# Performance work log

Hardware: AMD Instinct MI355X
Metric: run time of the kernel (lower is better)

The kernel has to match this reference:

```python
import jax, jax.numpy as jnp
import numpy as np

B, N, D, E, FF, TOP_K = 4, 1024, 1024, 8, 4096, 2

def setup_inputs() -> dict:
    key = jax.random.key(0)
    ks = jax.random.split(key, 6)
    s = lambda k, shape: (jax.random.normal(k, shape, jnp.float32) * 0.02)
    x  = jax.random.normal(ks[0], (B, N, D), jnp.float32)
    Wr = s(ks[1], (E, D))            # router: logits = x @ Wr.T (no bias)
    W1 = s(ks[2], (E, D, FF)); b1 = jnp.zeros((E, FF), jnp.float32)  # fc1
    Wg = s(ks[3], (E, D, FF)); bg = jnp.zeros((E, FF), jnp.float32)  # fc_gate
    W2 = s(ks[4], (E, FF, D)); b2 = jnp.zeros((E, D), jnp.float32)   # fc2
    return {"x": x, "Wr": Wr, "W1": W1, "b1": b1, "Wg": Wg, "bg": bg, "W2": W2, "b2": b2}

def reference(x, Wr, W1, b1, Wg, bg, W2, b2):
    Bb, Nn, Dd = x.shape
    xf = x.reshape(-1, Dd)                      # [T, D]
    T = xf.shape[0]
    logits = xf @ Wr.T                          # [T, E]
    probs = jax.nn.softmax(logits, axis=-1)
    topv, topi = jax.lax.top_k(probs, TOP_K)    # [T, K]
    topv = topv / (topv.sum(-1, keepdims=True) + 1e-6)
    # per-(expert,token) combine weight: comb[t, e] = sum_k topv[t,k] * (topi[t,k]==e)
    comb = jnp.zeros((T, E), x.dtype).at[jnp.arange(T)[:, None], topi].add(topv)
    # scan over experts (fixed small E) to keep memory to one [T, FF] at a time
    def step(acc, p):
        w1, bb1, wg, bbg, w2, bb2, we = p       # we: [T]
        h = xf @ w1 + bb1                       # [T, FF]
        g = xf @ wg + bbg
        out = (jax.nn.silu(g) * h) @ w2 + bb2   # [T, D]
        return acc + we[:, None] * out, None
    acc, _ = jax.lax.scan(step, jnp.zeros((T, Dd), x.dtype), (W1, b1, Wg, bg, W2, b2, comb.T))
    out_final = acc.reshape(Bb, Nn, Dd)
    # load-balance aux loss (computed under no_grad in torch)
    counts = jnp.zeros((E,), x.dtype).at[topi.reshape(-1)].add(1.0)
    frac = counts / (counts.sum() + 1e-6)
    lb = jax.lax.stop_gradient((frac * probs.sum(0)).sum() * E)
    return out_final, lb
```

## Files before the change

kernel.cpp:

```cpp
#include <hip/hip_runtime.h>
#include <hip/hip_bf16.h>
#include <math.h>

#define T_TOK 4096
#define D_DIM 1024
#define E_EXP 8
#define FF_DIM 4096
#define NROWS (T_TOK * 2)
#define MAXT1 40
#define MAXT2 72

typedef unsigned short u16;
typedef unsigned int u32;
typedef __attribute__((ext_vector_type(8))) short bf16x8;
typedef __attribute__((ext_vector_type(4))) float f32x4;
typedef __attribute__((ext_vector_type(2))) unsigned int u32x2;
typedef __attribute__((ext_vector_type(4))) short s16x4;

__device__ __forceinline__ u16 f2bf(float f) {
    union { float f; unsigned u; } v; v.f = f;
    unsigned r = v.u + 0x7FFFu + ((v.u >> 16) & 1u);
    return (u16)(r >> 16);
}

typedef const __attribute__((address_space(1))) u32* gas1_t;
typedef __attribute__((address_space(3))) u32* las3_t;
#define GLOAD16(g, l) __builtin_amdgcn_global_load_lds((gas1_t)(const void*)(g), (las3_t)(void*)(l), 16, 0, 0)
#define MFMA(a, b, c) __builtin_amdgcn_mfma_f32_16x16x32_bf16((a), (b), (c), 0, 0, 0)
#define CVTPK(dst, lo, hi) asm("v_cvt_pk_bf16_f32 %0, %1, %2" : "=v"(dst) : "v"(lo), "v"(hi))
#define CFENCE() asm volatile("" ::: "memory")
#define SIGB(r) (((r) ^ ((r) >> 2)) & 7)


__global__ __launch_bounds__(256) void k_router(
    const float* __restrict__ x, const float* __restrict__ Wr,
    u16* __restrict__ xbf,
    int* __restrict__ tok_e, float* __restrict__ tok_w,
    int* __restrict__ cnt, float* __restrict__ probsum)
{
    __shared__ float bp[E_EXP];
    __shared__ int   bc[E_EXP];
    const int tid = threadIdx.x;
    if (tid < E_EXP) { bp[tid] = 0.f; bc[tid] = 0; }
    __syncthreads();
    const int wave = tid >> 6, lane = tid & 63;
    const int t = blockIdx.x * 4 + wave;
    const float* xt = x + (size_t)t * D_DIM;
    u16* xo = xbf + (size_t)t * D_DIM;
    float a[E_EXP] = {0.f,0.f,0.f,0.f,0.f,0.f,0.f,0.f};
    for (int j = lane; j < D_DIM; j += 64) {
        float xv = xt[j];
        xo[j] = f2bf(xv);
        #pragma unroll
        for (int e = 0; e < E_EXP; e++) a[e] = fmaf(xv, Wr[e * D_DIM + j], a[e]);
    }
    #pragma unroll
    for (int e = 0; e < E_EXP; e++) {
        #pragma unroll
        for (int off = 32; off; off >>= 1) a[e] += __shfl_xor(a[e], off, 64);
    }
    if (lane == 0) {
        float mx = a[0];
        #pragma unroll
        for (int e = 1; e < E_EXP; e++) mx = fmaxf(mx, a[e]);
        float p[E_EXP], s = 0.f;
        #pragma unroll
        for (int e = 0; e < E_EXP; e++) { p[e] = expf(a[e] - mx); s += p[e]; }
        float inv = 1.f / s;
        #pragma unroll
        for (int e = 0; e < E_EXP; e++) { p[e] *= inv; atomicAdd(&bp[e], p[e]); }
        int e0 = 0; float v0 = p[0];
        #pragma unroll
        for (int e = 1; e < E_EXP; e++) if (p[e] > v0) { v0 = p[e]; e0 = e; }
        int e1 = -1; float v1 = -1.f;
        #pragma unroll
        for (int e = 0; e < E_EXP; e++) if (e != e0 && p[e] > v1) { v1 = p[e]; e1 = e; }
        float sv = v0 + v1 + 1e-6f;
        tok_e[2*t] = e0; tok_e[2*t+1] = e1;
        tok_w[2*t] = v0 / sv; tok_w[2*t+1] = v1 / sv;
        atomicAdd(&bc[e0], 1); atomicAdd(&bc[e1], 1);
    }
    __syncthreads();
    if (tid < E_EXP) { atomicAdd(&cnt[tid], bc[tid]); atomicAdd(&probsum[tid], bp[tid]); }
}

__global__ void k_prefix(const int* __restrict__ cnt, const float* __restrict__ probsum,
                         int* __restrict__ basep, int* __restrict__ cursor,
                         float* __restrict__ out_lb,
                         int* __restrict__ nt1, int* __restrict__ te1, int* __restrict__ tm1,
                         int* __restrict__ nt2, int* __restrict__ te2, int* __restrict__ tm2)
{
    if (threadIdx.x == 0) {
        int b = 0; float lb = 0.f;
        for (int e = 0; e < E_EXP; e++) {
            basep[e] = b; b += cnt[e];
            lb += ((float)cnt[e] / (8192.f + 1e-6f)) * probsum[e];
        }
        *out_lb = lb * (float)E_EXP;
        int n1 = 0, n2 = 0;
        for (int e = 0; e < E_EXP; e++) {
            for (int m = 0; m < cnt[e]; m += 256) { te1[n1] = e; tm1[n1] = m; n1++; }
            for (int m = 0; m < cnt[e]; m += 128) { te2[n2] = e; tm2[n2] = m; n2++; }
        }
        *nt1 = n1; *nt2 = n2;
    }
    if (threadIdx.x < E_EXP) cursor[threadIdx.x] = 0;
}

__global__ void k_assign(const int* __restrict__ tok_e, const float* __restrict__ tok_w,
                         const int* __restrict__ basep, int* __restrict__ cursor,
                         int* __restrict__ row_token, int* __restrict__ row_slot,
                         float* __restrict__ row_weight)
{
    int t = blockIdx.x * blockDim.x + threadIdx.x;
    if (t >= T_TOK) return;
    #pragma unroll
    for (int k = 0; k < 2; k++) {
        int e = tok_e[2*t + k];
        int pos = basep[e] + atomicAdd(&cursor[e], 1);
        row_token[pos] = t; row_slot[pos] = k; row_weight[pos] = tok_w[2*t + k];
    }
}

__global__ __launch_bounds__(256) void k_cvt_w2(const float* __restrict__ W2, u16* __restrict__ w2t,
                                                int* __restrict__ cnt, float* __restrict__ probsum) {
    __shared__ u16 t[64][68];
    if (blockIdx.x == 0 && blockIdx.y == 0 && blockIdx.z == 0 && threadIdx.x < E_EXP) {
        cnt[threadIdx.x] = 0; probsum[threadIdx.x] = 0.f;
    }
    const float* in = W2 + (size_t)blockIdx.z * FF_DIM * D_DIM;
    u16* out = w2t + (size_t)blockIdx.z * FF_DIM * D_DIM;
    const int R = FF_DIM, C = D_DIM;
    const int r0 = blockIdx.y * 64, c0 = blockIdx.x * 64;
    const int tid = threadIdx.x;
    const int lr = tid >> 4, lc = (tid & 15) * 4;
    #pragma unroll
    for (int i = 0; i < 4; i++) {
        const int r = lr + i * 16;
        f32x4 v = *(const f32x4*)(in + (size_t)(r0 + r) * C + c0 + lc);
        s16x4 w;
        #pragma unroll
        for (int j = 0; j < 4; j++) w[j] = (short)f2bf(v[j]);
        *(s16x4*)&t[r][lc] = w;
    }
    __syncthreads();
    #pragma unroll
    for (int i = 0; i < 4; i++) {
        const int c = lr + i * 16;
        s16x4 w;
        #pragma unroll
        for (int j = 0; j < 4; j++) w[j] = (short)t[lc + j][c];
        *(s16x4*)(out + (size_t)(c0 + c) * R + r0 + lc) = w;
    }
}


__global__ __launch_bounds__(512, 2) void k_pass1(
    const u16* __restrict__ xbf,
    const float* __restrict__ W1, const float* __restrict__ Wg,
    const float* __restrict__ b1v, const float* __restrict__ bgv,
    const int* __restrict__ cnt, const int* __restrict__ basep,
    const int* __restrict__ row_token,
    const int* __restrict__ ntp, const int* __restrict__ te, const int* __restrict__ tm,
    u16* __restrict__ hg)
{
    const int ty = blockIdx.y;
    if (ty >= *ntp) return;
    const int e = te[ty];
    const int m0 = tm[ty];
    const int count = cnt[e];
    const int rbase = basep[e];
    const int n0 = blockIdx.x * 128;

    __shared__ __align__(16) u16 LDS[2 * 32768];

    const int tid = threadIdx.x;
    const int l = tid & 63;
    const int w = tid >> 6;

    const int rb = tid >> 3;
    const int swA = ((tid & 7) ^ ((tid >> 3) & 7)) * 8;
    const u16* sA[4];
    #pragma unroll
    for (int s = 0; s < 4; s++) {
        int g = m0 + rb + s * 64; if (g > count - 1) g = count - 1;
        sA[s] = xbf + (size_t)row_token[rbase + g] * D_DIM + swA;
    }

    const int nq = tid & 31;
    const int kq = tid >> 5;
    const float* pBh = W1 + ((size_t)e * D_DIM + kq * 4) * FF_DIM + n0 + nq * 4;
    const float* pBg = Wg + ((size_t)e * D_DIM + kq * 4) * FF_DIM + n0 + nq * 4;
    const int cW = kq >> 1;
    const int offW = (kq & 1) * 4;
    int wdst[4];
    #pragma unroll
    for (int j = 0; j < 4; j++) {
        const int row = nq * 4 + j;
        wdst[j] = row * 64 + (cW ^ SIGB(row)) * 8 + offW;
    }

    const int wm = w >> 2, wn = w & 3;
    const int fr = l & 15, q = l >> 4;
    const int s7 = fr & 7;

    f32x4 acc_h[8][2], acc_g[8][2];
    const f32x4 z4 = {0.f, 0.f, 0.f, 0.f};
    #pragma unroll
    for (int mf = 0; mf < 8; mf++)
        #pragma unroll
        for (int nf = 0; nf < 2; nf++) { acc_h[mf][nf] = z4; acc_g[mf][nf] = z4; }

    f32x4 vb0, vb1, vb2, vb3;

    #define LOADB1(P, K0) do { \
        const float* p_ = (P) + (size_t)(K0) * FF_DIM; \
        vb0 = *(const f32x4*)(p_); \
        vb1 = *(const f32x4*)(p_ + FF_DIM); \
        vb2 = *(const f32x4*)(p_ + 2 * FF_DIM); \
        vb3 = *(const f32x4*)(p_ + 3 * FF_DIM); \
    } while (0)

    #define CVTW1(BASE) do { \
        _Pragma("unroll") \
        for (int j = 0; j < 4; j++) { \
            u32 lo_, hi_; u32x2 wv_; \
            CVTPK(lo_, vb0[j], vb1[j]); \
            CVTPK(hi_, vb2[j], vb3[j]); \
            wv_.x = lo_; wv_.y = hi_; \
            *(u32x2*)&LDS[(BASE) + wdst[j]] = wv_; \
        } \
    } while (0)

    #define STAGE_A1(B, K0) do { \
        _Pragma("unroll") \
        for (int s = 0; s < 4; s++) \
            GLOAD16(sA[s] + (K0), &LDS[(B) * 32768 + s * 4096 + tid * 8]); \
    } while (0)

    auto COMP = [&](int kk, int ab) {
        const int rsA = ((kk * 4 + q) ^ s7) * 8;
        const int rB0 = wn * 32 + fr, rB1 = wn * 32 + 16 + fr;
        const int cb0 = ((kk * 4 + q) ^ SIGB(rB0)) * 8;
        const int cb1 = ((kk * 4 + q) ^ SIGB(rB1)) * 8;
        bf16x8 bh0 = *(const bf16x8*)&LDS[ab + 16384 + rB0 * 64 + cb0];
        bf16x8 bg0 = *(const bf16x8*)&LDS[ab + 24576 + rB0 * 64 + cb0];
        bf16x8 bh1 = *(const bf16x8*)&LDS[ab + 16384 + rB1 * 64 + cb1];
        bf16x8 bg1 = *(const bf16x8*)&LDS[ab + 24576 + rB1 * 64 + cb1];
        #define LDA1(i) (*(const bf16x8*)&LDS[ab + (wm * 128 + (i) * 16 + fr) * 64 + rsA])
        #define MF4(areg, i) do { \
            __builtin_amdgcn_s_setprio(1); \
            acc_h[i][0] = MFMA(areg, bh0, acc_h[i][0]); \
            acc_h[i][1] = MFMA(areg, bh1, acc_h[i][1]); \
            acc_g[i][0] = MFMA(areg, bg0, acc_g[i][0]); \
            acc_g[i][1] = MFMA(areg, bg1, acc_g[i][1]); \
            __builtin_amdgcn_s_setprio(0); } while (0)
        bf16x8 aA = LDA1(0);
        bf16x8 aB = LDA1(1);
        bf16x8 aC;
        aC = LDA1(2); MF4(aA, 0);
        aA = LDA1(3); MF4(aB, 1);
        aB = LDA1(4); MF4(aC, 2);
        aC = LDA1(5); MF4(aA, 3);
        aA = LDA1(6); MF4(aB, 4);
        aB = LDA1(7); MF4(aC, 5);
        MF4(aA, 6);
        MF4(aB, 7);
        #undef LDA1
        #undef MF4
    };

    const int NT = D_DIM / 64;
    LOADB1(pBh, 0);
    CVTW1(0 + 16384);
    STAGE_A1(0, 0);
    LOADB1(pBg, 0);
    CVTW1(0 + 24576);
    asm volatile("s_waitcnt vmcnt(0) lgkmcnt(0)" ::: "memory");
    __builtin_amdgcn_s_barrier();
    CFENCE();

    int b = 0;
    #pragma unroll 1
    for (int t = 0; t < NT; ++t) {
        const int ab = b * 32768;
        const int nboff = (b ^ 1) * 32768;
        const int kN = (t + 1 < NT ? t + 1 : NT - 1) * 64;
        LOADB1(pBh, kN);
        COMP(0, ab);
        CVTW1(nboff + 16384);
        STAGE_A1(b ^ 1, kN);
        LOADB1(pBg, kN);
        COMP(1, ab);
        CVTW1(nboff + 24576);
        asm volatile("s_waitcnt vmcnt(0) lgkmcnt(0)" ::: "memory");
        __builtin_amdgcn_s_barrier();
        CFENCE();
        b ^= 1;
    }
    asm volatile("s_waitcnt vmcnt(0)" ::: "memory");
    #undef LOADB1
    #undef CVTW1
    #undef STAGE_A1

    const float* b1p = b1v + (size_t)e * FF_DIM + n0;
    const float* bgp = bgv + (size_t)e * FF_DIM + n0;
    #pragma unroll
    for (int mf = 0; mf < 8; mf++) {
        const int rl = wm * 128 + mf * 16 + q * 4;
        #pragma unroll
        for (int r = 0; r < 4; r++) {
            const int g = m0 + rl + r;
            if (g < count) {
                u16* orow = hg + (size_t)(rbase + g) * FF_DIM + n0;
                #pragma unroll
                for (int nf = 0; nf < 2; nf++) {
                    const int col = wn * 32 + nf * 16 + fr;
                    float hv = acc_h[mf][nf][r] + b1p[col];
                    float gv = acc_g[mf][nf][r] + bgp[col];
                    float sig = 1.f / (1.f + expf(-gv));
                    orow[col] = f2bf(gv * sig * hv);
                }
            }
        }
    }
}


__global__ __launch_bounds__(256, 2) void k_pass2(
    const u16* __restrict__ hg,
    const u16* __restrict__ w2t, const float* __restrict__ b2v,
    const int* __restrict__ cnt, const int* __restrict__ basep,
    const int* __restrict__ row_token, const int* __restrict__ row_slot,
    const float* __restrict__ row_weight,
    const int* __restrict__ ntp, const int* __restrict__ te, const int* __restrict__ tm,
    float* __restrict__ contrib)
{
    const int ty = blockIdx.y;
    if (ty >= *ntp) return;
    const int e = te[ty];
    const int m0 = tm[ty];
    const int count = cnt[e];
    const int rbase = basep[e];
    const int n0 = blockIdx.x * 128;

    __shared__ __align__(16) u16 LDS[2 * 16384];

    const int tid = threadIdx.x;
    const int l = tid & 63;
    const int w = tid >> 6;

    const int rb = tid >> 3;
    const int sw0 = ((tid & 7) ^ ((tid >> 3) & 7)) * 8;
    const u16* sA[4];
    #pragma unroll
    for (int s = 0; s < 4; s++) {
        int g = m0 + rb + s * 32; if (g > count - 1) g = count - 1;
        sA[s] = hg + (size_t)(rbase + g) * FF_DIM + sw0;
    }
    const u16* sB[4];
    #pragma unroll
    for (int s = 0; s < 4; s++)
        sB[s] = w2t + ((size_t)e * D_DIM + (size_t)(n0 + rb + s * 32)) * FF_DIM + sw0;

    const int wm = w >> 1, wn = w & 1;
    const int fr = l & 15, q = l >> 4;
    const int s7 = fr & 7;

    f32x4 acc[4][4];
    const f32x4 z4 = {0.f, 0.f, 0.f, 0.f};
    #pragma unroll
    for (int mf = 0; mf < 4; mf++)
        #pragma unroll
        for (int nf = 0; nf < 4; nf++) acc[mf][nf] = z4;

    auto STAGE = [&](int b, int k0) {
        #pragma unroll
        for (int s = 0; s < 4; s++)
            GLOAD16(sA[s] + k0, &LDS[b * 16384 + s * 2048 + tid * 8]);
        #pragma unroll
        for (int s = 0; s < 4; s++)
            GLOAD16(sB[s] + k0, &LDS[b * 16384 + 8192 + s * 2048 + tid * 8]);
    };

    const int NT = FF_DIM / 64;
    STAGE(0, 0);
    int cur = 0;
    #pragma unroll 1
    for (int t = 0; t < NT; ++t) {
        if (t + 1 < NT) {
            STAGE(cur ^ 1, (t + 1) * 64);
            asm volatile("s_waitcnt vmcnt(8)" ::: "memory");
        } else {
            asm volatile("s_waitcnt vmcnt(0)" ::: "memory");
        }
        __builtin_amdgcn_s_barrier();
        CFENCE();
        const int ab = cur * 16384;
        #pragma unroll
        for (int kk = 0; kk < 2; kk++) {
            const int rs = ((kk * 4 + q) ^ s7) * 8;
            bf16x8 a[4], bb[4];
            #pragma unroll
            for (int mf = 0; mf < 4; mf++)
                a[mf] = *(const bf16x8*)&LDS[ab + (wm * 64 + mf * 16 + fr) * 64 + rs];
            #pragma unroll
            for (int nf = 0; nf < 4; nf++)
                bb[nf] = *(const bf16x8*)&LDS[ab + 8192 + (wn * 64 + nf * 16 + fr) * 64 + rs];
            __builtin_amdgcn_s_setprio(1);
            #pragma unroll
            for (int mf = 0; mf < 4; mf++)
                #pragma unroll
                for (int nf = 0; nf < 4; nf++)
                    acc[mf][nf] = MFMA(a[mf], bb[nf], acc[mf][nf]);
            __builtin_amdgcn_s_setprio(0);
        }
        CFENCE();
        __builtin_amdgcn_s_barrier();
        cur ^= 1;
    }

    const float* b2p = b2v + (size_t)e * D_DIM + n0;
    #pragma unroll
    for (int mf = 0; mf < 4; mf++) {
        const int rl = wm * 64 + mf * 16 + q * 4;
        #pragma unroll
        for (int r = 0; r < 4; r++) {
            const int g = m0 + rl + r;
            if (g < count) {
                const int token = row_token[rbase + g];
                const int slot  = row_slot[rbase + g];
                const float wgt_ = row_weight[rbase + g];
                float* orow = contrib + ((size_t)slot * T_TOK + token) * D_DIM + n0;
                #pragma unroll
                for (int nf = 0; nf < 4; nf++) {
                    const int col = wn * 64 + nf * 16 + fr;
                    orow[col] = wgt_ * (acc[mf][nf][r] + b2p[col]);
                }
            }
        }
    }
}

__global__ void k_combine(const float* __restrict__ contrib, float* __restrict__ out) {
    int i = blockIdx.x * blockDim.x + threadIdx.x;
    const f32x4* c0 = (const f32x4*)contrib;
    const f32x4* c1 = c0 + ((size_t)T_TOK * D_DIM / 4);
    f32x4* o = (f32x4*)out;
    o[i] = c0[i] + c1[i];
}


extern "C" void kernel_launch(void* const* d_in, const int* in_sizes, int n_in,
                              void* d_out, int out_size, void* d_ws, size_t ws_size,
                              hipStream_t stream)
{
    (void)in_sizes; (void)n_in; (void)out_size; (void)ws_size;
    const float* x  = (const float*)d_in[0];
    const float* Wr = (const float*)d_in[1];
    const float* W1 = (const float*)d_in[2];
    const float* b1 = (const float*)d_in[3];
    const float* Wg = (const float*)d_in[4];
    const float* bg = (const float*)d_in[5];
    const float* W2 = (const float*)d_in[6];
    const float* b2 = (const float*)d_in[7];
    float* out = (float*)d_out;

    char* ws = (char*)d_ws;
    u16* xbf = (u16*)ws;             ws += (size_t)T_TOK * D_DIM * sizeof(u16);
    u16* w2t = (u16*)ws;             ws += (size_t)E_EXP * D_DIM * FF_DIM * sizeof(u16);
    u16* hg = (u16*)ws;              ws += (size_t)NROWS * FF_DIM * sizeof(u16);
    float* contrib = (float*)ws;     ws += (size_t)2 * T_TOK * D_DIM * sizeof(float);
    int* tok_e = (int*)ws;           ws += (size_t)T_TOK * 2 * sizeof(int);
    float* tok_w = (float*)ws;       ws += (size_t)T_TOK * 2 * sizeof(float);
    int* row_token = (int*)ws;       ws += (size_t)NROWS * sizeof(int);
    int* row_slot = (int*)ws;        ws += (size_t)NROWS * sizeof(int);
    float* row_weight = (float*)ws;  ws += (size_t)NROWS * sizeof(float);
    int* cnt = (int*)ws;             ws += 8 * sizeof(int);
    int* basep = (int*)ws;           ws += 8 * sizeof(int);
    int* cursor = (int*)ws;          ws += 8 * sizeof(int);
    float* probsum = (float*)ws;     ws += 8 * sizeof(float);
    int* nt1 = (int*)ws;             ws += sizeof(int);
    int* nt2 = (int*)ws;             ws += sizeof(int);
    int* te1 = (int*)ws;             ws += MAXT1 * sizeof(int);
    int* tm1 = (int*)ws;             ws += MAXT1 * sizeof(int);
    int* te2 = (int*)ws;             ws += MAXT2 * sizeof(int);
    int* tm2 = (int*)ws;             ws += MAXT2 * sizeof(int);

    k_cvt_w2<<<dim3(D_DIM / 64, FF_DIM / 64, E_EXP), 256, 0, stream>>>(W2, w2t, cnt, probsum);
    k_router<<<T_TOK / 4, 256, 0, stream>>>(x, Wr, xbf, tok_e, tok_w, cnt, probsum);
    k_prefix<<<1, 64, 0, stream>>>(cnt, probsum, basep, cursor, out + (size_t)T_TOK * D_DIM,
                                   nt1, te1, tm1, nt2, te2, tm2);
    k_assign<<<T_TOK / 256, 256, 0, stream>>>(tok_e, tok_w, basep, cursor, row_token, row_slot, row_weight);
    k_pass1<<<dim3(FF_DIM / 128, MAXT1), 512, 0, stream>>>(xbf, W1, Wg, b1, bg, cnt, basep, row_token,
                                                           nt1, te1, tm1, hg);
    k_pass2<<<dim3(D_DIM / 128, MAXT2), 256, 0, stream>>>(hg, w2t, b2, cnt, basep, row_token, row_slot, row_weight,
                                                          nt2, te2, tm2, contrib);
    k_combine<<<(T_TOK * D_DIM / 4) / 256, 256, 0, stream>>>(contrib, out);
}
```

Measured before the change: 460.0 us.

## Fuse router with W2 conversion and merge prefix/assign into one kernel

Merges the router and the W2 bf16 transpose-conversion into a single launch by giving them disjoint block ranges. Prefix and assign are folded into one single-block kernel that reduces per-block expert counts and scatters rows with shared-memory cursors. Global atomics and the counter reset are replaced by per-block partial arrays. This removes two kernel launches and the gaps between them. In exchange, the assign scatter for 4096 tokens now runs on a single block, which may be slower than the old multi-block version.

```diff
diff --git a/kernel.cpp b/kernel.cpp
--- a/kernel.cpp
+++ b/kernel.cpp
@@ -9,6 +9,8 @@
 #define NROWS (T_TOK * 2)
 #define MAXT1 40
 #define MAXT2 72
+#define NRBLK 1024
+#define NW2TILE 8192
 
 typedef unsigned short u16;
 typedef unsigned int u32;
@@ -31,126 +33,151 @@
 #define CFENCE() asm volatile("" ::: "memory")
 #define SIGB(r) (((r) ^ ((r) >> 2)) & 7)
 
-
-__global__ __launch_bounds__(256) void k_router(
+__global__ __launch_bounds__(256) void k_front(
     const float* __restrict__ x, const float* __restrict__ Wr,
     u16* __restrict__ xbf,
     int* __restrict__ tok_e, float* __restrict__ tok_w,
-    int* __restrict__ cnt, float* __restrict__ probsum)
+    int* __restrict__ blk_cnt, float* __restrict__ blk_ps,
+    const float* __restrict__ W2, u16* __restrict__ w2t)
 {
-    __shared__ float bp[E_EXP];
-    __shared__ int   bc[E_EXP];
     const int tid = threadIdx.x;
-    if (tid < E_EXP) { bp[tid] = 0.f; bc[tid] = 0; }
+    const int bid = blockIdx.x;
+
+    if (bid < NRBLK) {
+        __shared__ float bp[E_EXP];
+        __shared__ int   bc[E_EXP];
+        if (tid < E_EXP) { bp[tid] = 0.f; bc[tid] = 0; }
+        __syncthreads();
+        const int wave = tid >> 6, lane = tid & 63;
+        const int t = bid * 4 + wave;
+        const float* xt = x + (size_t)t * D_DIM;
+        u16* xo = xbf + (size_t)t * D_DIM;
+        float a[E_EXP] = {0.f,0.f,0.f,0.f,0.f,0.f,0.f,0.f};
+        for (int j = lane; j < D_DIM; j += 64) {
+            float xv = xt[j];
+            xo[j] = f2bf(xv);
+            #pragma unroll
+            for (int e = 0; e < E_EXP; e++) a[e] = fmaf(xv, Wr[e * D_DIM + j], a[e]);
+        }
+        #pragma unroll
+        for (int e = 0; e < E_EXP; e++) {
+            #pragma unroll
+            for (int off = 32; off; off >>= 1) a[e] += __shfl_xor(a[e], off, 64);
+        }
+        if (lane == 0) {
+            float mx = a[0];
+            #pragma unroll
+            for (int e = 1; e < E_EXP; e++) mx = fmaxf(mx, a[e]);
+            float p[E_EXP], s = 0.f;
+            #pragma unroll
+            for (int e = 0; e < E_EXP; e++) { p[e] = expf(a[e] - mx); s += p[e]; }
+            float inv = 1.f / s;
+            #pragma unroll
+            for (int e = 0; e < E_EXP; e++) { p[e] *= inv; atomicAdd(&bp[e], p[e]); }
+            int e0 = 0; float v0 = p[0];
+            #pragma unroll
+            for (int e = 1; e < E_EXP; e++) if (p[e] > v0) { v0 = p[e]; e0 = e; }
+            int e1 = -1; float v1 = -1.f;
+            #pragma unroll
+            for (int e = 0; e < E_EXP; e++) if (e != e0 && p[e] > v1) { v1 = p[e]; e1 = e; }
+            float sv = v0 + v1 + 1e-6f;
+            tok_e[2*t] = e0; tok_e[2*t+1] = e1;
+            tok_w[2*t] = v0 / sv; tok_w[2*t+1] = v1 / sv;
+            atomicAdd(&bc[e0], 1); atomicAdd(&bc[e1], 1);
+        }
+        __syncthreads();
+        if (tid < E_EXP) {
+            blk_cnt[bid * E_EXP + tid] = bc[tid];
+            blk_ps[bid * E_EXP + tid]  = bp[tid];
+        }
+    } else {
+        __shared__ u16 tbuf[64][68];
+        const int tile = bid - NRBLK;
+        const int e2 = tile >> 10;
+        const int rem = tile & 1023;
+        const int r0 = (rem >> 4) * 64;
+        const int c0 = (rem & 15) * 64;
+        const float* in = W2 + ((size_t)e2 * FF_DIM + r0) * D_DIM + c0;
+        u16* out = w2t + ((size_t)e2 * D_DIM + c0) * FF_DIM + r0;
+        const int lr = tid >> 4, lc = (tid & 15) * 4;
+        #pragma unroll
+        for (int i = 0; i < 4; i++) {
+            const int r = lr + i * 16;
+            f32x4 v = *(const f32x4*)(in + (size_t)r * D_DIM + lc);
+            s16x4 w;
+            #pragma unroll
+            for (int j = 0; j < 4; j++) w[j] = (short)f2bf(v[j]);
+            *(s16x4*)&tbuf[r][lc] = w;
+        }
+        __syncthreads();
+        #pragma unroll
+        for (int i = 0; i < 4; i++) {
+            const int c = lr + i * 16;
+            s16x4 w;
+            #pragma unroll
+            for (int j = 0; j < 4; j++) w[j] = (short)tbuf[lc + j][c];
+            *(s16x4*)(out + (size_t)c * FF_DIM + lc) = w;
+        }
+    }
+}
+
+__global__ __launch_bounds__(256) void k_prefix_assign(
+    const int* __restrict__ blk_cnt, const float* __restrict__ blk_ps,
+    const int* __restrict__ tok_e, const float* __restrict__ tok_w,
+    int* __restrict__ cnt, int* __restrict__ basep,
+    float* __restrict__ out_lb,
+    int* __restrict__ nt1, int* __restrict__ te1, int* __restrict__ tm1,
+    int* __restrict__ nt2, int* __restrict__ te2, int* __restrict__ tm2,
+    int* __restrict__ row_token, int* __restrict__ row_slot,
+    float* __restrict__ row_weight)
+{
+    __shared__ int   s_cnt[E_EXP];
+    __shared__ int   s_base[E_EXP];
+    __shared__ int   s_cur[E_EXP];
+    const int tid = threadIdx.x;
+
+    const int e = tid >> 5, lane32 = tid & 31;
+    int ce = 0; float pe = 0.f;
+    for (int b = lane32; b < NRBLK; b += 32) {
+        ce += blk_cnt[b * E_EXP + e];
+        pe += blk_ps[b * E_EXP + e];
+    }
+    #pragma unroll
+    for (int off = 16; off; off >>= 1) {
+        ce += __shfl_xor(ce, off, 32);
+        pe += __shfl_xor(pe, off, 32);
+    }
+    __shared__ float s_ps[E_EXP];
+    if (lane32 == 0) { s_cnt[e] = ce; s_ps[e] = pe; }
+    if (tid < E_EXP) s_cur[tid] = 0;
     __syncthreads();
-    const int wave = tid >> 6, lane = tid & 63;
-    const int t = blockIdx.x * 4 + wave;
-    const float* xt = x + (size_t)t * D_DIM;
-    u16* xo = xbf + (size_t)t * D_DIM;
-    float a[E_EXP] = {0.f,0.f,0.f,0.f,0.f,0.f,0.f,0.f};
-    for (int j = lane; j < D_DIM; j += 64) {
-        float xv = xt[j];
-        xo[j] = f2bf(xv);
-        #pragma unroll
-        for (int e = 0; e < E_EXP; e++) a[e] = fmaf(xv, Wr[e * D_DIM + j], a[e]);
-    }
-    #pragma unroll
-    for (int e = 0; e < E_EXP; e++) {
-        #pragma unroll
-        for (int off = 32; off; off >>= 1) a[e] += __shfl_xor(a[e], off, 64);
-    }
-    if (lane == 0) {
-        float mx = a[0];
-        #pragma unroll
-        for (int e = 1; e < E_EXP; e++) mx = fmaxf(mx, a[e]);
-        float p[E_EXP], s = 0.f;
-        #pragma unroll
-        for (int e = 0; e < E_EXP; e++) { p[e] = expf(a[e] - mx); s += p[e]; }
-        float inv = 1.f / s;
-        #pragma unroll
-        for (int e = 0; e < E_EXP; e++) { p[e] *= inv; atomicAdd(&bp[e], p[e]); }
-        int e0 = 0; float v0 = p[0];
-        #pragma unroll
-        for (int e = 1; e < E_EXP; e++) if (p[e] > v0) { v0 = p[e]; e0 = e; }
-        int e1 = -1; float v1 = -1.f;
-        #pragma unroll
-        for (int e = 0; e < E_EXP; e++) if (e != e0 && p[e] > v1) { v1 = p[e]; e1 = e; }
-        float sv = v0 + v1 + 1e-6f;
-        tok_e[2*t] = e0; tok_e[2*t+1] = e1;
-        tok_w[2*t] = v0 / sv; tok_w[2*t+1] = v1 / sv;
-        atomicAdd(&bc[e0], 1); atomicAdd(&bc[e1], 1);
-    }
-    __syncthreads();
-    if (tid < E_EXP) { atomicAdd(&cnt[tid], bc[tid]); atomicAdd(&probsum[tid], bp[tid]); }
-}
-
-__global__ void k_prefix(const int* __restrict__ cnt, const float* __restrict__ probsum,
-                         int* __restrict__ basep, int* __restrict__ cursor,
-                         float* __restrict__ out_lb,
-                         int* __restrict__ nt1, int* __restrict__ te1, int* __restrict__ tm1,
-                         int* __restrict__ nt2, int* __restrict__ te2, int* __restrict__ tm2)
-{
-    if (threadIdx.x == 0) {
+
+    if (tid == 0) {
         int b = 0; float lb = 0.f;
-        for (int e = 0; e < E_EXP; e++) {
-            basep[e] = b; b += cnt[e];
-            lb += ((float)cnt[e] / (8192.f + 1e-6f)) * probsum[e];
+        for (int k = 0; k < E_EXP; k++) {
+            s_base[k] = b;
+            basep[k] = b;
+            cnt[k] = s_cnt[k];
+            lb += ((float)s_cnt[k] / (8192.f + 1e-6f)) * s_ps[k];
+            b += s_cnt[k];
         }
         *out_lb = lb * (float)E_EXP;
         int n1 = 0, n2 = 0;
-        for (int e = 0; e < E_EXP; e++) {
-            for (int m = 0; m < cnt[e]; m += 256) { te1[n1] = e; tm1[n1] = m; n1++; }
-            for (int m = 0; m < cnt[e]; m += 128) { te2[n2] = e; tm2[n2] = m; n2++; }
+        for (int k = 0; k < E_EXP; k++) {
+            for (int m = 0; m < s_cnt[k]; m += 256) { te1[n1] = k; tm1[n1] = m; n1++; }
+            for (int m = 0; m < s_cnt[k]; m += 128) { te2[n2] = k; tm2[n2] = m; n2++; }
         }
         *nt1 = n1; *nt2 = n2;
     }
-    if (threadIdx.x < E_EXP) cursor[threadIdx.x] = 0;
-}
-
-__global__ void k_assign(const int* __restrict__ tok_e, const float* __restrict__ tok_w,
-                         const int* __restrict__ basep, int* __restrict__ cursor,
-                         int* __restrict__ row_token, int* __restrict__ row_slot,
-                         float* __restrict__ row_weight)
-{
-    int t = blockIdx.x * blockDim.x + threadIdx.x;
-    if (t >= T_TOK) return;
-    #pragma unroll
-    for (int k = 0; k < 2; k++) {
-        int e = tok_e[2*t + k];
-        int pos = basep[e] + atomicAdd(&cursor[e], 1);
-        row_token[pos] = t; row_slot[pos] = k; row_weight[pos] = tok_w[2*t + k];
-    }
-}
-
-__global__ __launch_bounds__(256) void k_cvt_w2(const float* __restrict__ W2, u16* __restrict__ w2t,
-                                                int* __restrict__ cnt, float* __restrict__ probsum) {
-    __shared__ u16 t[64][68];
-    if (blockIdx.x == 0 && blockIdx.y == 0 && blockIdx.z == 0 && threadIdx.x < E_EXP) {
-        cnt[threadIdx.x] = 0; probsum[threadIdx.x] = 0.f;
-    }
-    const float* in = W2 + (size_t)blockIdx.z * FF_DIM * D_DIM;
-    u16* out = w2t + (size_t)blockIdx.z * FF_DIM * D_DIM;
-    const int R = FF_DIM, C = D_DIM;
-    const int r0 = blockIdx.y * 64, c0 = blockIdx.x * 64;
-    const int tid = threadIdx.x;
-    const int lr = tid >> 4, lc = (tid & 15) * 4;
-    #pragma unroll
-    for (int i = 0; i < 4; i++) {
-        const int r = lr + i * 16;
-        f32x4 v = *(const f32x4*)(in + (size_t)(r0 + r) * C + c0 + lc);
-        s16x4 w;
-        #pragma unroll
-        for (int j = 0; j < 4; j++) w[j] = (short)f2bf(v[j]);
-        *(s16x4*)&t[r][lc] = w;
-    }
     __syncthreads();
-    #pragma unroll
-    for (int i = 0; i < 4; i++) {
-        const int c = lr + i * 16;
-        s16x4 w;
-        #pragma unroll
-        for (int j = 0; j < 4; j++) w[j] = (short)t[lc + j][c];
-        *(s16x4*)(out + (size_t)(c0 + c) * R + r0 + lc) = w;
+
+    for (int t = tid; t < T_TOK; t += 256) {
+        #pragma unroll
+        for (int k = 0; k < 2; k++) {
+            int ex = tok_e[2*t + k];
+            int pos = s_base[ex] + atomicAdd(&s_cur[ex], 1);
+            row_token[pos] = t; row_slot[pos] = k; row_weight[pos] = tok_w[2*t + k];
+        }
     }
 }
 
@@ -476,10 +503,10 @@
     int* row_token = (int*)ws;       ws += (size_t)NROWS * sizeof(int);
     int* row_slot = (int*)ws;        ws += (size_t)NROWS * sizeof(int);
     float* row_weight = (float*)ws;  ws += (size_t)NROWS * sizeof(float);
+    int* blk_cnt = (int*)ws;         ws += (size_t)NRBLK * E_EXP * sizeof(int);
+    float* blk_ps = (float*)ws;      ws += (size_t)NRBLK * E_EXP * sizeof(float);
     int* cnt = (int*)ws;             ws += 8 * sizeof(int);
     int* basep = (int*)ws;           ws += 8 * sizeof(int);
-    int* cursor = (int*)ws;          ws += 8 * sizeof(int);
-    float* probsum = (float*)ws;     ws += 8 * sizeof(float);
     int* nt1 = (int*)ws;             ws += sizeof(int);
     int* nt2 = (int*)ws;             ws += sizeof(int);
     int* te1 = (int*)ws;             ws += MAXT1 * sizeof(int);
@@ -487,11 +514,12 @@
     int* te2 = (int*)ws;             ws += MAXT2 * sizeof(int);
     int* tm2 = (int*)ws;             ws += MAXT2 * sizeof(int);
 
-    k_cvt_w2<<<dim3(D_DIM / 64, FF_DIM / 64, E_EXP), 256, 0, stream>>>(W2, w2t, cnt, probsum);
-    k_router<<<T_TOK / 4, 256, 0, stream>>>(x, Wr, xbf, tok_e, tok_w, cnt, probsum);
-    k_prefix<<<1, 64, 0, stream>>>(cnt, probsum, basep, cursor, out + (size_t)T_TOK * D_DIM,
-                                   nt1, te1, tm1, nt2, te2, tm2);
-    k_assign<<<T_TOK / 256, 256, 0, stream>>>(tok_e, tok_w, basep, cursor, row_token, row_slot, row_weight);
+    k_front<<<NRBLK + NW2TILE, 256, 0, stream>>>(x, Wr, xbf, tok_e, tok_w,
+                                                 blk_cnt, blk_ps, W2, w2t);
+    k_prefix_assign<<<1, 256, 0, stream>>>(blk_cnt, blk_ps, tok_e, tok_w,
+                                           cnt, basep, out + (size_t)T_TOK * D_DIM,
+                                           nt1, te1, tm1, nt2, te2, tm2,
+                                           row_token, row_slot, row_weight);
     k_pass1<<<dim3(FF_DIM / 128, MAXT1), 512, 0, stream>>>(xbf, W1, Wg, b1, bg, cnt, basep, row_token,
                                                            nt1, te1, tm1, hg);
     k_pass2<<<dim3(D_DIM / 128, MAXT2), 256, 0, stream>>>(hg, w2t, b2, cnt, basep, row_token, row_slot, row_weight,
```

Result: faster. 411.5 us (-10.5%).
